# Optimization experiments

Hardware: AMD Instinct MI355X
Metric: run time of the kernel (lower is better)

The kernel has to match this reference:

```python
import jax, jax.numpy as jnp
import numpy as np

D = 1024
NHEAD = 16
HEAD_DIM = D // NHEAD


def setup_inputs() -> dict:
    key = jax.random.key(0)
    ks = jax.random.split(key, 7)
    B, L = 4, 2048
    q = jax.random.normal(ks[0], (B, L, D), dtype=jnp.float32)
    k = jax.random.normal(ks[1], (B, L, D), dtype=jnp.float32)
    v = jax.random.normal(ks[2], (B, L, D), dtype=jnp.float32)
    # packed QKV projection, as in nn.MultiheadAttention (in_proj_weight: [3d, d])
    scale = 1.0 / np.sqrt(D)
    in_proj_w = jax.random.uniform(ks[3], (3 * D, D), dtype=jnp.float32, minval=-scale, maxval=scale)
    in_proj_b = jnp.zeros((3 * D,), dtype=jnp.float32)
    out_w = jax.random.uniform(ks[4], (D, D), dtype=jnp.float32, minval=-scale, maxval=scale)
    out_b = jnp.zeros((D,), dtype=jnp.float32)
    return {"q": q, "k": k, "v": v, "in_proj_w": in_proj_w, "in_proj_b": in_proj_b,
            "out_w": out_w, "out_b": out_b}


def reference(q, k, v, in_proj_w, in_proj_b, out_w, out_b):
    # FP32 MHA, need_weights=True (average over heads), eval mode (dropout inactive).
    B, Lq, d = q.shape
    Lk = k.shape[1]
    # packed in-projection: rows [0:d] -> Q, [d:2d] -> K, [2d:3d] -> V
    qp = q @ in_proj_w[:d].T + in_proj_b[:d]
    kp = k @ in_proj_w[d:2 * d].T + in_proj_b[d:2 * d]
    vp = v @ in_proj_w[2 * d:].T + in_proj_b[2 * d:]
    # split heads: [B, H, L, hd]
    qp = qp.reshape(B, Lq, NHEAD, HEAD_DIM).transpose(0, 2, 1, 3)
    kp = kp.reshape(B, Lk, NHEAD, HEAD_DIM).transpose(0, 2, 1, 3)
    vp = vp.reshape(B, Lk, NHEAD, HEAD_DIM).transpose(0, 2, 1, 3)
    scores = jnp.einsum('bhqd,bhkd->bhqk', qp, kp) / jnp.sqrt(jnp.float32(HEAD_DIM))
    attn = jax.nn.softmax(scores, axis=-1)          # [B, H, Lq, Lk]
    ctx = jnp.einsum('bhqk,bhkd->bhqd', attn, vp)    # [B, H, Lq, hd]
    ctx = ctx.transpose(0, 2, 1, 3).reshape(B, Lq, d)
    out = ctx @ out_w.T + out_b                      # [B, Lq, d]
    weights = attn.mean(axis=1)                      # average over heads -> [B, Lq, Lk]
    return out, weights
```

## Files before the change

kernel.cpp:

```cpp
#include <hip/hip_runtime.h>
#include <hip/hip_bf16.h>

#define D_ 1024
#define NH 16
#define HD 64
#define B_ 4
#define L_ 2048
#define N_ (B_*L_)
#define BH_ (B_*NH)
#define QSCALE_ 0.18033688011112042f

typedef __bf16 bf16_t;
typedef __bf16 bf16x4 __attribute__((ext_vector_type(4)));
typedef __bf16 bf16x8 __attribute__((ext_vector_type(8)));
typedef float f32x4 __attribute__((ext_vector_type(4)));

typedef const __attribute__((address_space(1))) char gas_t;
typedef __attribute__((address_space(3))) char las_t;

__device__ __forceinline__ f32x4 mfma_bf16(bf16x8 a, bf16x8 b, f32x4 c) {
    return __builtin_amdgcn_mfma_f32_16x16x32_bf16(a, b, c, 0, 0, 0);
}

__device__ __forceinline__ bf16x8 cvt8_f32(const float* __restrict__ p) {
    const float4* p4 = reinterpret_cast<const float4*>(p);
    float4 a = p4[0], b = p4[1];
    bf16x8 r;
    r[0] = (bf16_t)a.x; r[1] = (bf16_t)a.y; r[2] = (bf16_t)a.z; r[3] = (bf16_t)a.w;
    r[4] = (bf16_t)b.x; r[5] = (bf16_t)b.y; r[6] = (bf16_t)b.z; r[7] = (bf16_t)b.w;
    return r;
}

__device__ __forceinline__ bf16x8 ld8_bf16(const bf16_t* __restrict__ p) {
    return *reinterpret_cast<const bf16x8*>(p);
}

__global__ __launch_bounds__(256) void k_cvt_all(
    const float* __restrict__ s0, const float* __restrict__ s1,
    const float* __restrict__ s2, const float* __restrict__ sw,
    const float* __restrict__ so,
    bf16_t* __restrict__ d0, bf16_t* __restrict__ d1, bf16_t* __restrict__ d2,
    bf16_t* __restrict__ dw, bf16_t* __restrict__ dow)
{
    const int n8  = N_ * D_ / 8;
    const int n8w = 3 * D_ * D_ / 8;
    const int n8o = D_ * D_ / 8;
    const int tot = 3 * n8 + n8w + n8o;
    int i = blockIdx.x * blockDim.x + threadIdx.x;
    int stride = gridDim.x * blockDim.x;
    for (; i < tot; i += stride) {
        const float* s; bf16_t* d; int off;
        if (i < 3 * n8) {
            int seg = i >> 20; off = i & (n8 - 1);
            s = (seg == 0) ? s0 : ((seg == 1) ? s1 : s2);
            d = (seg == 0) ? d0 : ((seg == 1) ? d1 : d2);
        } else if (i < 3 * n8 + n8w) {
            off = i - 3 * n8; s = sw; d = dw;
        } else {
            off = i - 3 * n8 - n8w; s = so; d = dow;
        }
        *reinterpret_cast<bf16x8*>(d + (size_t)off * 8) = cvt8_f32(s + (size_t)off * 8);
    }
}

__global__ __launch_bounds__(256, 4) void k_gemm_qkv(
    const bf16_t* __restrict__ qb, const bf16_t* __restrict__ kb,
    const bf16_t* __restrict__ vb, const bf16_t* __restrict__ wb,
    const float* __restrict__ bias,
    bf16_t* __restrict__ qp, bf16_t* __restrict__ kp, bf16_t* __restrict__ vpT)
{
    __shared__ __align__(16) char ldsA[2][8192];
    __shared__ __align__(16) char ldsB[2][8192];
    int tid  = threadIdx.x;
    int lane = tid & 63, w = tid >> 6;
    int r = lane & 15, g = lane >> 4;
    int wr = w >> 1, wc = w & 1;

    int bid   = blockIdx.x;
    int xcd   = bid & 7;
    int seq   = bid >> 3;
    int sec   = seq >> 6;
    int inner = seq & 63;
    int tm  = xcd * 8 + (inner >> 3);
    int ctl = (inner & 7) * 128;

    const bf16_t* A = (sec == 0) ? qb : ((sec == 1) ? kb : vb);
    const bf16_t* Ab = A + (size_t)tm * 128 * 1024;
    const bf16_t* Bb = wb + (size_t)sec * D_ * D_ + (size_t)ctl * 1024;

    f32x4 z = {0.f, 0.f, 0.f, 0.f};
    f32x4 acc[4][4];
    #pragma unroll
    for (int m = 0; m < 4; ++m)
        #pragma unroll
        for (int n = 0; n < 4; ++n) acc[m][n] = z;

    auto stage = [&](int buf, int k0) {
        #pragma unroll
        for (int i = 0; i < 2; ++i) {
            int idx = i * 256 + tid;
            int row = idx >> 2;
            int lc  = (idx & 3) ^ ((row >> 1) & 3);
            const bf16_t* gA = Ab + (size_t)row * 1024 + k0 + lc * 8;
            const bf16_t* gB = Bb + (size_t)row * 1024 + k0 + lc * 8;
            __builtin_amdgcn_global_load_lds((gas_t*)gA,
                (las_t*)(&ldsA[buf][0] + idx * 16), 16, 0, 0);
            __builtin_amdgcn_global_load_lds((gas_t*)gB,
                (las_t*)(&ldsB[buf][0] + idx * 16), 16, 0, 0);
        }
    };

    stage(0, 0);
    stage(1, 32);
    int buf = 0;

    for (int k0 = 0; k0 < 1024; k0 += 32) {
        if (k0 < 992) asm volatile("s_waitcnt vmcnt(4)" ::: "memory");
        else          asm volatile("s_waitcnt vmcnt(0)" ::: "memory");
        __builtin_amdgcn_s_barrier();
        __builtin_amdgcn_sched_barrier(0);

        bf16x8 af[4], bf_[4];
        #pragma unroll
        for (int m = 0; m < 4; ++m) {
            int R = wr * 64 + m * 16 + r;
            af[m] = *reinterpret_cast<const bf16x8*>(
                &ldsA[buf][0] + R * 64 + (((g ^ ((R >> 1) & 3)) << 4)));
        }
        #pragma unroll
        for (int n = 0; n < 4; ++n) {
            int R = wc * 64 + n * 16 + r;
            bf_[n] = *reinterpret_cast<const bf16x8*>(
                &ldsB[buf][0] + R * 64 + (((g ^ ((R >> 1) & 3)) << 4)));
        }
        #pragma unroll
        for (int m = 0; m < 4; ++m)
            #pragma unroll
            for (int n = 0; n < 4; ++n)
                acc[m][n] = mfma_bf16(af[m], bf_[n], acc[m][n]);

        __builtin_amdgcn_s_barrier();
        if (k0 + 64 < 1024) stage(buf, k0 + 64);
        buf ^= 1;
    }

    #pragma unroll
    for (int m = 0; m < 4; ++m)
        #pragma unroll
        for (int n = 0; n < 4; ++n)
            #pragma unroll
            for (int i = 0; i < 4; ++i) {
                int row = tm * 128 + wr * 64 + m * 16 + g * 4 + i;
                int col = ctl + wc * 64 + n * 16 + r;
                float val = acc[m][n][i] + bias[sec * 1024 + col];
                int bb = row >> 11, ln = row & 2047;
                int h = col >> 6, dd = col & 63;
                if (sec == 0)
                    qp[(((size_t)(bb * NH + h)) * L_ + ln) * HD + dd] =
                        (bf16_t)(val * QSCALE_);
                else if (sec == 1)
                    kp[(((size_t)(bb * NH + h)) * L_ + ln) * HD + dd] = (bf16_t)val;
                else
                    vpT[(((size_t)(bb * NH + h)) * HD + dd) * L_ + ln] = (bf16_t)val;
            }
}

__global__ __launch_bounds__(256, 4) void k_attn(
    const bf16_t* __restrict__ qp, const bf16_t* __restrict__ kp,
    const bf16_t* __restrict__ vpT,
    bf16_t* __restrict__ ctx, float* __restrict__ lInvOut)
{
    __shared__ __align__(16) char sK[8192];
    __shared__ __align__(16) char sV[8192];
    __shared__ __align__(16) char sP[4][4096];

    int tid  = threadIdx.x;
    int w    = tid >> 6;
    int lane = tid & 63;
    int r = lane & 15, g = lane >> 4;
    int bh = blockIdx.x & 63;
    int qg = blockIdx.x >> 6;
    int qbase = qg * 128 + w * 32;

    const bf16_t* qpb = qp  + (size_t)bh * L_ * HD;
    const bf16_t* kpb = kp  + (size_t)bh * L_ * HD;
    const bf16_t* vtb = vpT + (size_t)bh * HD * L_;

    bf16x8 bq[2][2];
    #pragma unroll
    for (int qt = 0; qt < 2; ++qt)
        #pragma unroll
        for (int ds = 0; ds < 2; ++ds)
            bq[qt][ds] = ld8_bf16(qpb + (size_t)(qbase + qt * 16 + r) * HD + ds * 32 + g * 8);

    bf16x8 ones;
    #pragma unroll
    for (int i = 0; i < 8; ++i) ones[i] = (bf16_t)1.0f;

    f32x4 z = {0.f, 0.f, 0.f, 0.f};
    f32x4 acc[2][4];
    #pragma unroll
    for (int qt = 0; qt < 2; ++qt)
        #pragma unroll
        for (int dt = 0; dt < 4; ++dt) acc[qt][dt] = z;
    f32x4 acc_l[2];
    acc_l[0] = z; acc_l[1] = z;

    char* Pw = &sP[w][0];

    int srow = tid >> 3;
    int slc  = (tid & 7) ^ (srow & 7);
    const bf16_t* gK0 = kpb + (size_t)srow * HD + slc * 8;
    const bf16_t* gV0 = vtb + (size_t)srow * L_ + slc * 8;

    for (int kt = 0; kt < 32; ++kt) {
        int k0 = kt * 64;
        const bf16_t* gK = gK0 + (size_t)k0 * HD;
        const bf16_t* gV = gV0 + k0;
        #pragma unroll
        for (int i = 0; i < 2; ++i) {
            __builtin_amdgcn_global_load_lds((gas_t*)(gK + (size_t)i * 32 * HD),
                (las_t*)(&sK[0] + i * 4096 + tid * 16), 16, 0, 0);
            __builtin_amdgcn_global_load_lds((gas_t*)(gV + (size_t)i * 32 * L_),
                (las_t*)(&sV[0] + i * 4096 + tid * 16), 16, 0, 0);
        }
        __syncthreads();

        f32x4 sT[4][2];
        __builtin_amdgcn_s_setprio(1);
        #pragma unroll
        for (int ktile = 0; ktile < 4; ++ktile) {
            bf16x8 a0 = *reinterpret_cast<const bf16x8*>(
                &sK[0] + (ktile * 16 + r) * 128 + (((g    ) ^ (r & 7)) << 4));
            bf16x8 a1 = *reinterpret_cast<const bf16x8*>(
                &sK[0] + (ktile * 16 + r) * 128 + (((4 + g) ^ (r & 7)) << 4));
            #pragma unroll
            for (int qt = 0; qt < 2; ++qt) {
                f32x4 t = mfma_bf16(a0, bq[qt][0], z);
                sT[ktile][qt] = mfma_bf16(a1, bq[qt][1], t);
            }
        }
        __builtin_amdgcn_s_setprio(0);

        #pragma unroll
        for (int qt = 0; qt < 2; ++qt) {
            #pragma unroll
            for (int ktile = 0; ktile < 4; ++ktile) {
                bf16x4 pw;
                #pragma unroll
                for (int i = 0; i < 4; ++i)
                    pw[i] = (bf16_t)__builtin_amdgcn_exp2f(sT[ktile][qt][i]);
                *reinterpret_cast<bf16x4*>(Pw + (qt * 16 + r) * 128 +
                    (((2 * ktile + (g >> 1)) ^ (r & 7)) << 4) + ((g & 1) << 3)) = pw;
            }
        }

        bf16x8 pa[2][2];
        #pragma unroll
        for (int qt = 0; qt < 2; ++qt)
            #pragma unroll
            for (int ks = 0; ks < 2; ++ks)
                pa[qt][ks] = *reinterpret_cast<const bf16x8*>(
                    Pw + (qt * 16 + r) * 128 + (((4 * ks + g) ^ (r & 7)) << 4));
        __builtin_amdgcn_s_setprio(1);
        #pragma unroll
        for (int qt = 0; qt < 2; ++qt) {
            acc_l[qt] = mfma_bf16(pa[qt][0], ones, acc_l[qt]);
            acc_l[qt] = mfma_bf16(pa[qt][1], ones, acc_l[qt]);
        }
        #pragma unroll
        for (int dt = 0; dt < 4; ++dt)
            #pragma unroll
            for (int ks = 0; ks < 2; ++ks) {
                bf16x8 bv = *reinterpret_cast<const bf16x8*>(
                    &sV[0] + (dt * 16 + r) * 128 + (((4 * ks + g) ^ (r & 7)) << 4));
                acc[0][dt] = mfma_bf16(pa[0][ks], bv, acc[0][dt]);
                acc[1][dt] = mfma_bf16(pa[1][ks], bv, acc[1][dt]);
            }
        __builtin_amdgcn_s_setprio(0);

        __syncthreads();
    }

    int bb = bh >> 4, h = bh & 15;
    #pragma unroll
    for (int qt = 0; qt < 2; ++qt) {
        float lq[4];
        #pragma unroll
        for (int i = 0; i < 4; ++i) lq[i] = 1.0f / acc_l[qt][i];
        #pragma unroll
        for (int i = 0; i < 4; ++i) {
            int q = qbase + qt * 16 + 4 * g + i;
            #pragma unroll
            for (int dt = 0; dt < 4; ++dt) {
                float val = acc[qt][dt][i] * lq[i];
                ctx[(((size_t)(bb * L_ + q)) * NH + h) * HD + dt * 16 + r] = (bf16_t)val;
            }
        }
        if (r == 0) {
            #pragma unroll
            for (int i = 0; i < 4; ++i) {
                int q = qbase + qt * 16 + 4 * g + i;
                lInvOut[(size_t)bh * L_ + q] = lq[i];
            }
        }
    }
}

__global__ __launch_bounds__(256, 2) void k_wo(
    const bf16_t* __restrict__ qp, const bf16_t* __restrict__ kp,
    const float* __restrict__ lInv, float* __restrict__ wout,
    const bf16_t* __restrict__ ctxA, const bf16_t* __restrict__ owb,
    const float* __restrict__ obias, float* __restrict__ outp)
{
    __shared__ __align__(16) char smem[73728];

    int tid  = threadIdx.x;
    int w    = tid >> 6;
    int lane = tid & 63;
    int r = lane & 15, g = lane >> 4;
    int wr = w >> 1, wc = w & 1;

    int bid   = blockIdx.x;
    int third = bid % 3;
    int grp   = bid / 3;
    f32x4 z = {0.f, 0.f, 0.f, 0.f};

    if (third < 2) {
        int wi = grp * 2 + third;
        char*  sQm  = smem;
        char*  sKm  = smem + 32768;
        float* sLi  = (float*)(smem + 65536);

        int wgid = (wi & 7) * 128 + (wi >> 3);
        int chunk = wgid >> 7;
        int b  = chunk >> 1;
        int qh = chunk & 1;
        int rem = wgid & 127;
        int qt = qh * 8 + (rem >> 4);
        int kt = rem & 15;
        int q0 = qt * 128, k0 = kt * 128;

        #pragma unroll
        for (int i = 0; i < 2; ++i) {
            int idx = i * 256 + tid;
            int h   = idx >> 5;
            int off = (idx & 31) * 4;
            const float* gl = lInv + ((size_t)(b * NH + h) * L_ + q0 + off);
            __builtin_amdgcn_global_load_lds((gas_t*)gl,
                (las_t*)((char*)sLi + i * 4096 + w * 1024), 16, 0, 0);
        }

        auto stage_qk = [&](int buf, int h) {
            const bf16_t* Qh = qp + ((size_t)(b * NH + h) * L_ + q0) * HD;
            const bf16_t* Kh = kp + ((size_t)(b * NH + h) * L_ + k0) * HD;
            #pragma unroll
            for (int i = 0; i < 4; ++i) {
                int idx = i * 256 + tid;
                int row = idx >> 3;
                int lc  = (idx & 7) ^ (row & 7);
                const bf16_t* gQ = Qh + (size_t)row * HD + lc * 8;
                const bf16_t* gK = Kh + (size_t)row * HD + lc * 8;
                __builtin_amdgcn_global_load_lds((gas_t*)gQ,
                    (las_t*)(sQm + buf * 16384 + i * 4096 + w * 1024), 16, 0, 0);
                __builtin_amdgcn_global_load_lds((gas_t*)gK,
                    (las_t*)(sKm + buf * 16384 + i * 4096 + w * 1024), 16, 0, 0);
            }
        };

        float acc[4][4][4] = {};
        stage_qk(0, 0);
        __syncthreads();
        int buf = 0;

        for (int h = 0; h < NH; ++h) {
            if (h + 1 < NH) stage_qk(buf ^ 1, h + 1);

            const char* Qb = sQm + buf * 16384;
            const char* Kb = sKm + buf * 16384;

            bf16x8 bfrag[4][2];
            #pragma unroll
            for (int nf = 0; nf < 4; ++nf) {
                int R = wc * 64 + nf * 16 + r;
                bfrag[nf][0] = *reinterpret_cast<const bf16x8*>(
                    Kb + R * 128 + (((g    ) ^ (R & 7)) << 4));
                bfrag[nf][1] = *reinterpret_cast<const bf16x8*>(
                    Kb + R * 128 + (((4 + g) ^ (R & 7)) << 4));
            }
            #pragma unroll
            for (int mf = 0; mf < 4; ++mf) {
                int R = wr * 64 + mf * 16 + r;
                bf16x8 af0 = *reinterpret_cast<const bf16x8*>(
                    Qb + R * 128 + (((g    ) ^ (R & 7)) << 4));
                bf16x8 af1 = *reinterpret_cast<const bf16x8*>(
                    Qb + R * 128 + (((4 + g) ^ (R & 7)) << 4));
                int qrow = wr * 64 + mf * 16 + g * 4;
                f32x4 liv = *reinterpret_cast<const f32x4*>(&sLi[qrow] + h * 128);
                #pragma unroll
                for (int nf = 0; nf < 4; ++nf) {
                    f32x4 t = mfma_bf16(af0, bfrag[nf][0], z);
                    t = mfma_bf16(af1, bfrag[nf][1], t);
                    #pragma unroll
                    for (int i = 0; i < 4; ++i)
                        acc[mf][nf][i] += __builtin_amdgcn_exp2f(t[i]) * liv[i];
                }
            }
            __syncthreads();
            buf ^= 1;
        }

        const float inv_h = 1.0f / (float)NH;
        #pragma unroll
        for (int mf = 0; mf < 4; ++mf)
            #pragma unroll
            for (int nf = 0; nf < 4; ++nf)
                #pragma unroll
                for (int i = 0; i < 4; ++i) {
                    int qidx = q0 + wr * 64 + mf * 16 + g * 4 + i;
                    int kidx = k0 + wc * 64 + nf * 16 + r;
                    wout[((size_t)(b * L_ + qidx)) * L_ + kidx] = acc[mf][nf][i] * inv_h;
                }
    } else {
        int oi = grp;
        char* ldsA0 = smem;
        char* ldsB0 = smem + 16384;

        int swz = (oi & 7) * 64 + (oi >> 3);
        int tm = swz >> 3, tn = swz & 7;

        const bf16_t* Ab = ctxA + (size_t)tm * 128 * 1024;
        const bf16_t* Bb = owb  + (size_t)tn * 128 * 1024;

        f32x4 acc[4][4];
        #pragma unroll
        for (int m = 0; m < 4; ++m)
            #pragma unroll
            for (int n = 0; n < 4; ++n) acc[m][n] = z;

        auto stage = [&](int buf, int k0) {
            #pragma unroll
            for (int i = 0; i < 2; ++i) {
                int idx = i * 256 + tid;
                int row = idx >> 2;
                int lc  = (idx & 3) ^ ((row >> 1) & 3);
                const bf16_t* gA = Ab + (size_t)row * 1024 + k0 + lc * 8;
                const bf16_t* gB = Bb + (size_t)row * 1024 + k0 + lc * 8;
                __builtin_amdgcn_global_load_lds((gas_t*)gA,
                    (las_t*)(ldsA0 + buf * 8192 + idx * 16), 16, 0, 0);
                __builtin_amdgcn_global_load_lds((gas_t*)gB,
                    (las_t*)(ldsB0 + buf * 8192 + idx * 16), 16, 0, 0);
            }
        };

        stage(0, 0);
        stage(1, 32);
        int buf = 0;

        for (int k0 = 0; k0 < 1024; k0 += 32) {
            if (k0 < 992) asm volatile("s_waitcnt vmcnt(4)" ::: "memory");
            else          asm volatile("s_waitcnt vmcnt(0)" ::: "memory");
            __builtin_amdgcn_s_barrier();
            __builtin_amdgcn_sched_barrier(0);

            bf16x8 af[4], bf_[4];
            #pragma unroll
            for (int m = 0; m < 4; ++m) {
                int R = wr * 64 + m * 16 + r;
                af[m] = *reinterpret_cast<const bf16x8*>(
                    ldsA0 + buf * 8192 + R * 64 + (((g ^ ((R >> 1) & 3)) << 4)));
            }
            #pragma unroll
            for (int n = 0; n < 4; ++n) {
                int R = wc * 64 + n * 16 + r;
                bf_[n] = *reinterpret_cast<const bf16x8*>(
                    ldsB0 + buf * 8192 + R * 64 + (((g ^ ((R >> 1) & 3)) << 4)));
            }
            #pragma unroll
            for (int m = 0; m < 4; ++m)
                #pragma unroll
                for (int n = 0; n < 4; ++n)
                    acc[m][n] = mfma_bf16(af[m], bf_[n], acc[m][n]);

            __builtin_amdgcn_s_barrier();
            if (k0 + 64 < 1024) stage(buf, k0 + 64);
            buf ^= 1;
        }

        #pragma unroll
        for (int m = 0; m < 4; ++m)
            #pragma unroll
            for (int n = 0; n < 4; ++n)
                #pragma unroll
                for (int i = 0; i < 4; ++i) {
                    int row = tm * 128 + wr * 64 + m * 16 + g * 4 + i;
                    int col = tn * 128 + wc * 64 + n * 16 + r;
                    outp[(size_t)row * 1024 + col] = acc[m][n][i] + obias[col];
                }
    }
}

extern "C" void kernel_launch(void* const* d_in, const int* in_sizes, int n_in,
                              void* d_out, int out_size, void* d_ws, size_t ws_size,
                              hipStream_t stream) {
    const float* q     = (const float*)d_in[0];
    const float* k     = (const float*)d_in[1];
    const float* v     = (const float*)d_in[2];
    const float* in_w  = (const float*)d_in[3];
    const float* in_b  = (const float*)d_in[4];
    const float* out_w = (const float*)d_in[5];
    const float* out_b = (const float*)d_in[6];

    char* ws = (char*)d_ws;
    bf16_t* xb   = (bf16_t*)(ws);
    bf16_t* wb   = (bf16_t*)(ws + ((size_t)48 << 20));
    bf16_t* owb  = (bf16_t*)(ws + ((size_t)54 << 20));
    bf16_t* qp   = (bf16_t*)(ws + ((size_t)56 << 20));
    bf16_t* kp   = (bf16_t*)(ws + ((size_t)72 << 20));
    bf16_t* vpT  = (bf16_t*)(ws + ((size_t)88 << 20));
    bf16_t* ctx  = (bf16_t*)(ws + ((size_t)104 << 20));
    float*  lBuf = (float*)(ws + ((size_t)120 << 20));

    bf16_t* qb = xb;
    bf16_t* kb = xb + (size_t)N_ * D_;
    bf16_t* vb = xb + (size_t)2 * N_ * D_;

    float* outp = (float*)d_out;
    float* wout = outp + (size_t)N_ * D_;

    k_cvt_all<<<2048, 256, 0, stream>>>(q, k, v, in_w, out_w, qb, kb, vb, wb, owb);

    k_gemm_qkv<<<1536, 256, 0, stream>>>(qb, kb, vb, wb, in_b, qp, kp, vpT);

    k_attn<<<1024, 256, 0, stream>>>(qp, kp, vpT, ctx, lBuf);

    k_wo<<<1536, 256, 0, stream>>>(qp, kp, lBuf, wout, ctx, owb, out_b, outp);
}
```

Baseline: 263.0 us.

## Single-buffer QK staging in weights kernel to raise occupancy and remap blocks

Drops double buffering of the Q/K tiles in the head-averaged attention-weights branch, cutting LDS from 72KB to 40KB and raising launch bounds to 4 blocks per CU. It also changes the block-to-tile mapping to a period-of-24 scheme that interleaves weight and output-projection tiles with an XCD-aware assignment. The intent is more concurrent blocks to hide latency and better L2 locality per XCD. In exchange each head iteration now waits synchronously on its loads with no intra-block prefetch, and the higher occupancy target may force register spills given the 64-float accumulator.

```diff
diff --git a/kernel.cpp b/kernel.cpp
--- a/kernel.cpp
+++ b/kernel.cpp
@@ -307,13 +307,13 @@
     }
 }
 
-__global__ __launch_bounds__(256, 2) void k_wo(
+__global__ __launch_bounds__(256, 4) void k_wo(
     const bf16_t* __restrict__ qp, const bf16_t* __restrict__ kp,
     const float* __restrict__ lInv, float* __restrict__ wout,
     const bf16_t* __restrict__ ctxA, const bf16_t* __restrict__ owb,
     const float* __restrict__ obias, float* __restrict__ outp)
 {
-    __shared__ __align__(16) char smem[73728];
+    __shared__ __align__(16) char smem[40960];
 
     int tid  = threadIdx.x;
     int w    = tid >> 6;
@@ -321,24 +321,22 @@
     int r = lane & 15, g = lane >> 4;
     int wr = w >> 1, wc = w & 1;
 
-    int bid   = blockIdx.x;
-    int third = bid % 3;
-    int grp   = bid / 3;
+    int bid    = blockIdx.x;
+    int period = bid / 24;
+    int p      = bid % 24;
     f32x4 z = {0.f, 0.f, 0.f, 0.f};
 
-    if (third < 2) {
-        int wi = grp * 2 + third;
-        char*  sQm  = smem;
-        char*  sKm  = smem + 32768;
-        float* sLi  = (float*)(smem + 65536);
-
-        int wgid = (wi & 7) * 128 + (wi >> 3);
-        int chunk = wgid >> 7;
+    if (p < 16) {
+        int chunk  = p & 7;
+        int within = period * 2 + (p >> 3);
+        char*  sQm = smem;
+        char*  sKm = smem + 16384;
+        float* sLi = (float*)(smem + 32768);
+
         int b  = chunk >> 1;
         int qh = chunk & 1;
-        int rem = wgid & 127;
-        int qt = qh * 8 + (rem >> 4);
-        int kt = rem & 15;
+        int qt = qh * 8 + (within >> 4);
+        int kt = within & 15;
         int q0 = qt * 128, k0 = kt * 128;
 
         #pragma unroll
@@ -351,7 +349,7 @@
                 (las_t*)((char*)sLi + i * 4096 + w * 1024), 16, 0, 0);
         }
 
-        auto stage_qk = [&](int buf, int h) {
+        auto stage_qk = [&](int h) {
             const bf16_t* Qh = qp + ((size_t)(b * NH + h) * L_ + q0) * HD;
             const bf16_t* Kh = kp + ((size_t)(b * NH + h) * L_ + k0) * HD;
             #pragma unroll
@@ -362,41 +360,36 @@
                 const bf16_t* gQ = Qh + (size_t)row * HD + lc * 8;
                 const bf16_t* gK = Kh + (size_t)row * HD + lc * 8;
                 __builtin_amdgcn_global_load_lds((gas_t*)gQ,
-                    (las_t*)(sQm + buf * 16384 + i * 4096 + w * 1024), 16, 0, 0);
+                    (las_t*)(sQm + i * 4096 + w * 1024), 16, 0, 0);
                 __builtin_amdgcn_global_load_lds((gas_t*)gK,
-                    (las_t*)(sKm + buf * 16384 + i * 4096 + w * 1024), 16, 0, 0);
+                    (las_t*)(sKm + i * 4096 + w * 1024), 16, 0, 0);
             }
         };
 
         float acc[4][4][4] = {};
-        stage_qk(0, 0);
-        __syncthreads();
-        int buf = 0;
 
         for (int h = 0; h < NH; ++h) {
-            if (h + 1 < NH) stage_qk(buf ^ 1, h + 1);
-
-            const char* Qb = sQm + buf * 16384;
-            const char* Kb = sKm + buf * 16384;
+            stage_qk(h);
+            __syncthreads();
 
             bf16x8 bfrag[4][2];
             #pragma unroll
             for (int nf = 0; nf < 4; ++nf) {
                 int R = wc * 64 + nf * 16 + r;
                 bfrag[nf][0] = *reinterpret_cast<const bf16x8*>(
-                    Kb + R * 128 + (((g    ) ^ (R & 7)) << 4));
+                    sKm + R * 128 + (((g    ) ^ (R & 7)) << 4));
                 bfrag[nf][1] = *reinterpret_cast<const bf16x8*>(
-                    Kb + R * 128 + (((4 + g) ^ (R & 7)) << 4));
+                    sKm + R * 128 + (((4 + g) ^ (R & 7)) << 4));
             }
             #pragma unroll
             for (int mf = 0; mf < 4; ++mf) {
                 int R = wr * 64 + mf * 16 + r;
                 bf16x8 af0 = *reinterpret_cast<const bf16x8*>(
-                    Qb + R * 128 + (((g    ) ^ (R & 7)) << 4));
+                    sQm + R * 128 + (((g    ) ^ (R & 7)) << 4));
                 bf16x8 af1 = *reinterpret_cast<const bf16x8*>(
-                    Qb + R * 128 + (((4 + g) ^ (R & 7)) << 4));
+                    sQm + R * 128 + (((4 + g) ^ (R & 7)) << 4));
                 int qrow = wr * 64 + mf * 16 + g * 4;
-                f32x4 liv = *reinterpret_cast<const f32x4*>(&sLi[qrow] + h * 128);
+                f32x4 liv = *reinterpret_cast<const f32x4*>(sLi + h * 128 + qrow);
                 #pragma unroll
                 for (int nf = 0; nf < 4; ++nf) {
                     f32x4 t = mfma_bf16(af0, bfrag[nf][0], z);
@@ -407,7 +400,6 @@
                 }
             }
             __syncthreads();
-            buf ^= 1;
         }
 
         const float inv_h = 1.0f / (float)NH;
@@ -422,12 +414,13 @@
                     wout[((size_t)(b * L_ + qidx)) * L_ + kidx] = acc[mf][nf][i] * inv_h;
                 }
     } else {
-        int oi = grp;
+        int xcd = p - 16;
+        int ow  = period;
         char* ldsA0 = smem;
         char* ldsB0 = smem + 16384;
 
-        int swz = (oi & 7) * 64 + (oi >> 3);
-        int tm = swz >> 3, tn = swz & 7;
+        int tm = xcd * 8 + (ow >> 3);
+        int tn = ow & 7;
 
         const bf16_t* Ab = ctxA + (size_t)tm * 128 * 1024;
         const bf16_t* Bb = owb  + (size_t)tn * 128 * 1024;
```

After: 290.4 us. 1.1x slower.
